# Performance work log

Measured on AMD Instinct MI355X. Metric: run time of the kernel, lower is better.

The kernel has to match this reference:

```python
import jax, jax.numpy as jnp
import numpy as np

B, N, E, HD, L, LH, NC = 256, 96, 1024, 300, 2, 600, 7

def prelu(x, a):
    return jnp.where(x >= 0, x, a * x)

def setup_inputs():
    key = jax.random.key(0)
    ks = jax.random.split(key, 16)
    s = 0.02
    r = lambda i, shp: jax.random.normal(ks[i], shp, jnp.float32) * s
    z = lambda shp: jnp.zeros(shp, jnp.float32)
    GD = HD * (L + 1)
    inp = {}
    inp["features"] = jax.random.normal(ks[0], (B, N, E), jnp.float32)
    inp["s_mask"] = jax.random.randint(ks[1], (B, N, N), 0, 2, jnp.int32)
    inp["entro"] = jax.random.uniform(ks[2], (B, N), dtype=jnp.float32)
    inp["alpha"] = 0.5
    inp["threshold"] = 0.25
    inp["fc1_w"] = r(3, (HD, E)); inp["fc1_b"] = z((HD,))
    inp["gat_w"] = r(4, (L, 2 * HD)); inp["gat_b"] = z((L,))
    inp["wr0"] = r(5, (L, HD, HD)); inp["wr1"] = r(6, (L, HD, HD))
    inp["enhance_w"] = r(7, (E, E)); inp["enhance_b"] = z((E,))
    inp["prelu_a"] = jnp.array(0.25, jnp.float32)
    inp["lstm_w_ih"] = r(8, (4 * LH, E + GD)); inp["lstm_w_hh"] = r(9, (4 * LH, LH))
    inp["lstm_b_ih"] = z((4 * LH,)); inp["lstm_b_hh"] = z((4 * LH,))
    inp["mlp_w0"] = r(10, (HD, LH)); inp["mlp_b0"] = z((HD,)); inp["mlp_a0"] = jnp.array(0.25, jnp.float32)
    inp["mlp_w1"] = r(11, (HD, HD)); inp["mlp_b1"] = z((HD,)); inp["mlp_a1"] = jnp.array(0.25, jnp.float32)
    inp["out_w"] = r(12, (NC, HD)); inp["out_b"] = z((NC,))
    return inp

def reference(features, s_mask, entro, alpha, threshold, fc1_w, fc1_b, gat_w, gat_b, wr0, wr1, enhance_w, enhance_b, prelu_a, lstm_w_ih, lstm_w_hh, lstm_b_ih, lstm_b_hh, mlp_w0, mlp_b0, mlp_a0, mlp_w1, mlp_b1, mlp_a1, out_w, out_b):
    # context_filter: cosine similarity + entropy edge filtering -> binary adjacency (B,N,N)
    f = features / (jnp.linalg.norm(features, axis=-1, keepdims=True) + 1e-8)
    sim = jnp.einsum("bid,bjd->bij", f, f)
    comb = alpha * entro[:, None, :] + (1.0 - alpha) * sim
    adj = comb > threshold
    H0 = prelu(features @ fc1_w.T + fc1_b, prelu_a)
    sm = s_mask.astype(features.dtype)
    Hs = [H0]
    for l in range(L):
        Hl = Hs[-1]
        wq, wk = gat_w[l, :HD], gat_w[l, HD:]
        # fused GAT over all target nodes i: score[b,i,j] = wq.H[b,i] + wk.H[b,j] + b
        scores = (Hl @ wq)[:, :, None] + (Hl @ wk)[:, None, :] + gat_b[l]
        scores = jnp.where(adj, scores, -1e9)
        attn = jax.nn.softmax(scores, axis=-1)
        V0 = Hl @ wr0[l].T  # relation-0 transform
        V1 = Hl @ wr1[l].T  # relation-1 transform
        M = jnp.einsum("bij,bjd->bid", attn * sm, V0) + jnp.einsum("bij,bjd->bid", attn * (1.0 - sm), V1)
        Hs.append(M)
    Hcat = jnp.concatenate(Hs, axis=2)  # (B, N, HD*(L+1))
    feat = prelu(features @ enhance_w.T + enhance_b, prelu_a)
    seq = jnp.concatenate([feat, Hcat], axis=-1)
    zin = seq @ lstm_w_ih.T + lstm_b_ih + lstm_b_hh  # (B, N, 4*LH), input projection hoisted out of scan
    def step(carry, zt):
        h, c = carry
        g = zt + h @ lstm_w_hh.T
        i, fg, gg, o = jnp.split(g, 4, axis=-1)
        c = jax.nn.sigmoid(fg) * c + jax.nn.sigmoid(i) * jnp.tanh(gg)
        h = jax.nn.sigmoid(o) * jnp.tanh(c)
        return (h, c), h
    h0 = jnp.zeros((features.shape[0], LH), features.dtype)
    _, hs = jax.lax.scan(step, (h0, h0), jnp.swapaxes(zin, 0, 1))
    Hl = jnp.swapaxes(hs, 0, 1)  # (B, N, LH)
    x = prelu(Hl @ mlp_w0.T + mlp_b0, mlp_a0)
    x = prelu(x @ mlp_w1.T + mlp_b1, mlp_a1)
    return x @ out_w.T + out_b  # (B, N, NC)
```

## Files before the change

### kernel.cpp

```cpp
#include <hip/hip_runtime.h>
#include <cstdint>
#include <cstddef>

#define Bdim 256
#define Ndim 96
#define Edim 1024
#define HDdim 300
#define Ldim 2
#define LHdim 600
#define NCdim 7
#define GDdim 900
#define ROWS (Bdim*Ndim)
#define HSLICE 155648

typedef unsigned short u16;
typedef unsigned int   u32;
typedef float f32x4 __attribute__((ext_vector_type(4)));
typedef short bf16x8 __attribute__((ext_vector_type(8)));
typedef unsigned short u16x4 __attribute__((ext_vector_type(4)));

#define IDP 0x7FFFFFFF, 1, 30, 0, 0

__device__ inline u16 f2bf(float x) {
    u32 u = __builtin_bit_cast(u32, x);
    u32 r = (u + 0x7fffu + ((u >> 16) & 1u)) >> 16;
    return (u16)r;
}
__device__ inline float bf2f(u16 h) {
    u32 u = ((u32)h) << 16;
    return __builtin_bit_cast(float, u);
}

template<int OUT, int ACT>
__global__ __launch_bounds__(256) void gemm_bf16(
    const u16* __restrict__ Ah, int lda,
    const u16* __restrict__ Wh, int ldw,
    float* __restrict__ C, u16* __restrict__ Ch, int ldc,
    int M, int Nd, int K,
    const float* __restrict__ bias, const float* __restrict__ aptr)
{
    __shared__ u16 At[2][4][1024];
    __shared__ u16 Wt[2][4][1024];
    const int tid  = threadIdx.x;
    const int ny  = gridDim.y;
    const int nwg = gridDim.x * ny;
    const int lin = blockIdx.y * gridDim.x + blockIdx.x;
    const int q = nwg >> 3, r8 = nwg & 7;
    const int xcd = lin & 7, off = lin >> 3;
    const int swz = (xcd < r8) ? xcd * (q + 1) + off
                               : r8 * (q + 1) + (xcd - r8) * q + off;
    const int bm   = (swz / ny) * 128;
    const int bn   = (swz % ny) * 128;
    const int wv   = tid >> 6;
    const int lane = tid & 63;
    const int wr   = (wv >> 1) * 64;
    const int wc   = (wv & 1) * 64;
    const int l15  = lane & 15;
    const int kseg = lane >> 4;

    f32x4 acc[4][4];
    #pragma unroll
    for (int i = 0; i < 4; ++i)
        #pragma unroll
        for (int j = 0; j < 4; ++j) acc[i][j] = (f32x4){0.f,0.f,0.f,0.f};

    const int srow = tid & 127;
    const bool isA = (tid < 128);
    const int gr   = isA ? (bm + srow) : (bn + srow);
    const u16* pbase = (isA ? Ah : Wh) + (size_t)gr * (isA ? lda : ldw);
    u16* dst = isA ? &At[0][0][0] : &Wt[0][0][0];
    const int soff = srow * 8;

    bf16x8 rv[4];
    #pragma unroll
    for (int s = 0; s < 4; ++s) rv[s] = *(const bf16x8*)(pbase + s * 8);

    const int nk = K >> 5;
    for (int kc = 0; kc < nk; ++kc) {
        const int bufo = (kc & 1) << 12;
        #pragma unroll
        for (int s = 0; s < 4; ++s)
            *(bf16x8*)(dst + bufo + s * 1024 + soff) = rv[s];
        if (kc + 1 < nk) {
            const u16* p = pbase + (kc + 1) * 32;
            #pragma unroll
            for (int s = 0; s < 4; ++s) rv[s] = *(const bf16x8*)(p + s * 8);
        }
        __syncthreads();
        const u16* Ab = &At[0][0][0] + bufo + kseg * 1024;
        const u16* Wb = &Wt[0][0][0] + bufo + kseg * 1024;
        bf16x8 a[4], b[4];
        #pragma unroll
        for (int f = 0; f < 4; ++f) {
            a[f] = *(const bf16x8*)(Ab + (wr + f * 16 + l15) * 8);
            b[f] = *(const bf16x8*)(Wb + (wc + f * 16 + l15) * 8);
        }
        #pragma unroll
        for (int i = 0; i < 4; ++i)
            #pragma unroll
            for (int j = 0; j < 4; ++j)
                acc[i][j] = __builtin_amdgcn_mfma_f32_16x16x32_bf16(a[i], b[j], acc[i][j], 0, 0, 0);
    }

    const float av = (ACT == 1) ? *aptr : 0.f;
    const int r4 = (lane >> 4) * 4;
    #pragma unroll
    for (int j = 0; j < 4; ++j) {
        int col = bn + wc + j * 16 + l15;
        if (col >= Nd) continue;
        float bv = bias ? bias[col] : 0.f;
        #pragma unroll
        for (int i = 0; i < 4; ++i) {
            #pragma unroll
            for (int rr = 0; rr < 4; ++rr) {
                int row = bm + wr + i * 16 + r4 + rr;
                if (row >= M) continue;
                float v = acc[i][j][rr] + bv;
                if (ACT == 1) v = (v >= 0.f) ? v : av * v;
                if (OUT == 0) {
                    C[(size_t)row * ldc + col] = v;
                } else {
                    Ch[(size_t)row * ldc + col] = f2bf(v);
                }
            }
        }
    }
}

__global__ __launch_bounds__(256) void split_rows8(
    const float* __restrict__ src, int srcld,
    int pmask, int pmul1, int pshift, int pmul2, int padd,
    u16* __restrict__ dstH, int dstld,
    int wcols, int validK, int validRows)
{
    const int r = blockIdx.y * 4 + (threadIdx.x >> 6);
    const int c = (blockIdx.x * 64 + (threadIdx.x & 63)) * 8;
    if (c >= wcols) return;
    const int sr = (r & pmask) * pmul1 + (r >> pshift) * pmul2 + padd;
    const float* s = src + (size_t)sr * srcld;
    const bool rok = (r < validRows);
    float v[8];
    if (rok && c + 8 <= validK) {
        *(float4*)&v[0] = *(const float4*)(s + c);
        *(float4*)&v[4] = *(const float4*)(s + c + 4);
    } else {
        #pragma unroll
        for (int u = 0; u < 8; ++u) v[u] = (rok && c + u < validK) ? s[c + u] : 0.f;
    }
    bf16x8 H8;
    #pragma unroll
    for (int u = 0; u < 8; ++u) H8[u] = (short)f2bf(v[u]);
    *(bf16x8*)(dstH + (size_t)r * dstld + c) = H8;
}

__global__ __launch_bounds__(256) void bias_perm(
    const float* __restrict__ bih, const float* __restrict__ bhh, float* __restrict__ dst)
{
    int n = blockIdx.x * 256 + threadIdx.x;
    if (n >= 4 * LHdim) return;
    int o = (n & 3) * LHdim + (n >> 2);
    dst[n] = bih[o] + bhh[o];
}

__global__ __launch_bounds__(256) void wr_cat(
    const float* __restrict__ wr0, const float* __restrict__ wr1, float* __restrict__ dst)
{
    int c = blockIdx.x * 256 + threadIdx.x;
    if (c >= HDdim) return;
    int lr = blockIdx.y;
    int l = lr / (2 * HDdim), r = lr % (2 * HDdim);
    const float* src = (r < HDdim)
        ? wr0 + ((size_t)l * HDdim + r) * HDdim
        : wr1 + ((size_t)l * HDdim + (r - HDdim)) * HDdim;
    dst[(size_t)lr * HDdim + c] = src[c];
}

__global__ __launch_bounds__(256) void zero_range(float* __restrict__ p, int n)
{
    int i = blockIdx.x * 256 + threadIdx.x;
    if (i < n) p[i] = 0.f;
}

__global__ __launch_bounds__(256) void norm_kernel(const float* __restrict__ f, float* __restrict__ invn)
{
    int row  = blockIdx.x * 4 + (threadIdx.x >> 6);
    int lane = threadIdx.x & 63;
    const float* fr = f + (size_t)row * Edim;
    float ss = 0.f;
    for (int t = lane; t < Edim; t += 64) { float v = fr[t]; ss = fmaf(v, v, ss); }
    #pragma unroll
    for (int o = 32; o > 0; o >>= 1) ss += __shfl_down(ss, o);
    if (lane == 0) invn[row] = 1.f / (sqrtf(ss) + 1e-8f);
}

__global__ __launch_bounds__(256) void simadj_kernel(
    const float* __restrict__ f, const float* __restrict__ invn,
    const float* __restrict__ entro, const float* __restrict__ alphap,
    const float* __restrict__ thrp, uint8_t* __restrict__ adj)
{
    int b = blockIdx.x;
    __shared__ float S[16][100];
    int tid = threadIdx.x;
    int i0 = (tid >> 4) * 6, j0 = (tid & 15) * 6;
    float acc[6][6];
    #pragma unroll
    for (int i = 0; i < 6; ++i)
        #pragma unroll
        for (int j = 0; j < 6; ++j) acc[i][j] = 0.f;
    const float* fb = f + (size_t)b * Ndim * Edim;

    for (int k0 = 0; k0 < Edim; k0 += 16) {
        __syncthreads();
        #pragma unroll
        for (int r = 0; r < 6; ++r) {
            int n = (tid >> 4) + r * 16;
            S[tid & 15][n] = fb[(size_t)n * Edim + k0 + (tid & 15)];
        }
        __syncthreads();
        #pragma unroll
        for (int kk = 0; kk < 16; ++kk) {
            float a[6], bb[6];
            #pragma unroll
            for (int u = 0; u < 6; ++u) a[u] = S[kk][i0 + u];
            #pragma unroll
            for (int u = 0; u < 6; ++u) bb[u] = S[kk][j0 + u];
            #pragma unroll
            for (int i = 0; i < 6; ++i)
                #pragma unroll
                for (int j = 0; j < 6; ++j)
                    acc[i][j] = fmaf(a[i], bb[j], acc[i][j]);
        }
    }

    float alpha = *alphap, thr = *thrp;
    float onem = 1.f - alpha;
    #pragma unroll
    for (int i = 0; i < 6; ++i) {
        int ii = i0 + i;
        float inv_i = invn[b * Ndim + ii];
        #pragma unroll
        for (int j = 0; j < 6; ++j) {
            int jj = j0 + j;
            float simv = acc[i][j] * inv_i * invn[b * Ndim + jj];
            float comb = alpha * entro[b * Ndim + jj] + onem * simv;
            adj[((size_t)b * Ndim + ii) * Ndim + jj] = (comb > thr) ? 1 : 0;
        }
    }
}

__global__ __launch_bounds__(256) void k_kernel(
    const float* __restrict__ Hsrc, const float* __restrict__ wk,
    float* __restrict__ k)
{
    int row  = blockIdx.x * 4 + (threadIdx.x >> 6);
    int lane = threadIdx.x & 63;
    const float* h = Hsrc + (size_t)row * GDdim;
    float sk = 0.f;
    for (int t = lane; t < HDdim; t += 64) sk = fmaf(h[t], wk[t], sk);
    #pragma unroll
    for (int o = 32; o > 0; o >>= 1) sk += __shfl_down(sk, o);
    if (lane == 0) k[row] = sk;
}

__global__ __launch_bounds__(256) void gat_fused(
    const float* __restrict__ kbuf, const uint8_t* __restrict__ adj,
    const int* __restrict__ smask,
    const float* __restrict__ V,
    float* __restrict__ Mout)
{
    __shared__ u16 P0[96][100];
    __shared__ u16 P1[96][100];
    __shared__ u16 Vs0[96][96];
    __shared__ u16 Vs1[96][96];
    __shared__ float ek[96];
    __shared__ float rden[96];
    __shared__ float red[256];
    const int b = blockIdx.x;
    const int half = blockIdx.y;
    const int tid = threadIdx.x;

    float kj = (tid < Ndim) ? kbuf[tid * Bdim + b] : -1e30f;
    red[tid] = kj;
    __syncthreads();
    #pragma unroll
    for (int s = 128; s > 0; s >>= 1) {
        if (tid < s) red[tid] = fmaxf(red[tid], red[tid + s]);
        __syncthreads();
    }
    float kmax = red[0];
    if (tid < Ndim) ek[tid] = expf(kj - kmax);
    __syncthreads();
    if (tid < Ndim) {
        const uint8_t* ar = adj + ((size_t)b * Ndim + tid) * Ndim;
        float s = 0.f;
        for (int j = 0; j < Ndim; ++j) if (ar[j]) s += ek[j];
        rden[tid] = 1.f / s;
    }
    __syncthreads();
    for (int idx = tid; idx < Ndim * Ndim; idx += 256) {
        int i = idx / Ndim, j = idx - i * Ndim;
        float a = adj[((size_t)b * Ndim + i) * Ndim + j] ? ek[j] * rden[i] : 0.f;
        int s = smask[((size_t)b * Ndim + i) * Ndim + j];
        P0[i][j] = s ? f2bf(a) : (u16)0;
        P1[i][j] = s ? (u16)0 : f2bf(a);
    }
    __syncthreads();

    const int ti = tid >> 4, td = tid & 15;
    const int i0 = ti * 6, dbase = td * 6;
    for (int p = 2 * half; p < 2 * half + 2; ++p) {
        const int d0 = p * 96;
        const int dw = (p == 3) ? (HDdim - 288) : 96;
        for (int idx = tid; idx < 96 * 24; idx += 256) {
            int j = idx / 24, q4 = (idx - j * 24) * 4;
            if (q4 < dw) {
                size_t g = ((size_t)(j * Bdim + b)) * (2 * HDdim) + d0 + q4;
                float4 a = *(const float4*)(V + g);
                float4 c = *(const float4*)(V + g + HDdim);
                u16x4 ua = { f2bf(a.x), f2bf(a.y), f2bf(a.z), f2bf(a.w) };
                u16x4 uc = { f2bf(c.x), f2bf(c.y), f2bf(c.z), f2bf(c.w) };
                *(u16x4*)&Vs0[j][q4] = ua;
                *(u16x4*)&Vs1[j][q4] = uc;
            }
        }
        __syncthreads();
        float acc[6][6];
        #pragma unroll
        for (int ii = 0; ii < 6; ++ii)
            #pragma unroll
            for (int dd = 0; dd < 6; ++dd) acc[ii][dd] = 0.f;
        for (int j = 0; j < Ndim; j += 2) {
            float paj[6], pajn[6], pbj[6], pbjn[6];
            #pragma unroll
            for (int ii = 0; ii < 6; ++ii) {
                u32 w0 = *(const u32*)&P0[i0 + ii][j];
                u32 w1 = *(const u32*)&P1[i0 + ii][j];
                paj[ii]  = __builtin_bit_cast(float, w0 << 16);
                pajn[ii] = __builtin_bit_cast(float, w0 & 0xffff0000u);
                pbj[ii]  = __builtin_bit_cast(float, w1 << 16);
                pbjn[ii] = __builtin_bit_cast(float, w1 & 0xffff0000u);
            }
            float v0a[6], v0b[6], v1a[6], v1b[6];
            #pragma unroll
            for (int dd = 0; dd < 3; ++dd) {
                u32 wa = *(const u32*)&Vs0[j][dbase + 2 * dd];
                u32 wb = *(const u32*)&Vs0[j + 1][dbase + 2 * dd];
                u32 wc2 = *(const u32*)&Vs1[j][dbase + 2 * dd];
                u32 wd = *(const u32*)&Vs1[j + 1][dbase + 2 * dd];
                v0a[2*dd]   = __builtin_bit_cast(float, wa << 16);
                v0a[2*dd+1] = __builtin_bit_cast(float, wa & 0xffff0000u);
                v0b[2*dd]   = __builtin_bit_cast(float, wb << 16);
                v0b[2*dd+1] = __builtin_bit_cast(float, wb & 0xffff0000u);
                v1a[2*dd]   = __builtin_bit_cast(float, wc2 << 16);
                v1a[2*dd+1] = __builtin_bit_cast(float, wc2 & 0xffff0000u);
                v1b[2*dd]   = __builtin_bit_cast(float, wd << 16);
                v1b[2*dd+1] = __builtin_bit_cast(float, wd & 0xffff0000u);
            }
            #pragma unroll
            for (int ii = 0; ii < 6; ++ii)
                #pragma unroll
                for (int dd = 0; dd < 6; ++dd) {
                    acc[ii][dd] += paj[ii]  * v0a[dd] + pbj[ii]  * v1a[dd]
                                 + pajn[ii] * v0b[dd] + pbjn[ii] * v1b[dd];
                }
        }
        __syncthreads();
        #pragma unroll
        for (int ii = 0; ii < 6; ++ii) {
            #pragma unroll
            for (int dd = 0; dd < 6; ++dd) {
                int d = dbase + dd;
                if (d < dw)
                    Mout[((size_t)((i0 + ii) * Bdim + b)) * GDdim + d0 + d] = acc[ii][dd];
            }
        }
    }
}

__global__ __launch_bounds__(256) void lstm_bf16(
    const u16* __restrict__ hH,
    const float* __restrict__ cin,
    const u16* __restrict__ WH,
    const float* __restrict__ zt,
    u16* __restrict__ hHo,
    float* __restrict__ cout)
{
    __shared__ u16 As[2][4][256];
    __shared__ u16 Ws[2][4][512];
    __shared__ __align__(16) float gates[32][68];
    const int tid = threadIdx.x;
    const int bm = blockIdx.x * 32;
    const int bn = blockIdx.y * 64;
    const int wv = tid >> 6;
    const int lane = tid & 63;
    const int l15 = lane & 15;
    const int kseg = lane >> 4;
    const float4 fz = make_float4(0.f, 0.f, 0.f, 0.f);

    const int prow0 = tid >> 4,        pui0 = tid & 15;
    const int prow1 = (tid + 256) >> 4, pui1 = tid & 15;
    const int pn0 = bn + pui0 * 4,  pn1 = bn + pui1 * 4;
    const int pu0 = pn0 >> 2,       pu1 = pn1 >> 2;
    const bool ok0 = (pu0 < LHdim), ok1 = (pu1 < LHdim);
    const int bb0 = bm + prow0,     bb1 = bm + prow1;
    float4 z0 = ok0 ? *(const float4*)(zt + (size_t)bb0 * (4 * LHdim) + pn0) : fz;
    float4 z1 = ok1 ? *(const float4*)(zt + (size_t)bb1 * (4 * LHdim) + pn1) : fz;
    float ci0 = ok0 ? cin[bb0 * LHdim + pu0] : 0.f;
    float ci1 = ok1 ? cin[bb1 * LHdim + pu1] : 0.f;

    const int av = tid & 127;
    const int arow = av >> 2, akc = av & 3;
    const u16* asrc = hH + (size_t)(bm + arow) * 608 + akc * 8;
    const int aoff = akc * 256 + arow * 8;
    const bool doA = (tid < 128);
    const int wrow = tid >> 2, wkc = tid & 3;
    const u16* wsrc = WH + (size_t)(bn + wrow) * 608 + wkc * 8;
    const int woff2 = wrow * 8;

    f32x4 acc[2];
    acc[0] = (f32x4){0.f,0.f,0.f,0.f};
    acc[1] = (f32x4){0.f,0.f,0.f,0.f};

    bf16x8 ra = *(const bf16x8*)(asrc);
    bf16x8 rw = *(const bf16x8*)(wsrc);

    #pragma unroll
    for (int kc = 0; kc < 19; ++kc) {
        const int buf = kc & 1;
        if (doA) *(bf16x8*)(&As[buf][0][0] + aoff) = ra;
        *(bf16x8*)(&Ws[buf][wkc][woff2]) = rw;
        if (kc + 1 < 19) {
            ra = *(const bf16x8*)(asrc + (kc + 1) * 32);
            rw = *(const bf16x8*)(wsrc + (kc + 1) * 32);
        }
        __syncthreads();
        bf16x8 a0, a1, b;
        a0 = *(const bf16x8*)&As[buf][kseg][(l15) * 8];
        a1 = *(const bf16x8*)&As[buf][kseg][(16 + l15) * 8];
        b  = *(const bf16x8*)&Ws[buf][kseg][(wv * 16 + l15) * 8];
        acc[0] = __builtin_amdgcn_mfma_f32_16x16x32_bf16(a0, b, acc[0], 0, 0, 0);
        acc[1] = __builtin_amdgcn_mfma_f32_16x16x32_bf16(a1, b, acc[1], 0, 0, 0);
    }

    const int r4 = (lane >> 4) * 4;
    __syncthreads();
    #pragma unroll
    for (int i = 0; i < 2; ++i)
        #pragma unroll
        for (int rr = 0; rr < 4; ++rr)
            gates[i * 16 + r4 + rr][wv * 16 + l15] = acc[i][rr];
    __syncthreads();

    if (ok0) {
        float4 g = *(const float4*)&gates[prow0][pui0 * 4];
        float gi = g.x + z0.x;
        float gf = g.y + z0.y;
        float gg = g.z + z0.z;
        float go = g.w + z0.w;
        float si = 1.f / (1.f + expf(-gi));
        float sf = 1.f / (1.f + expf(-gf));
        float so = 1.f / (1.f + expf(-go));
        float cn = sf * ci0 + si * tanhf(gg);
        float hn = so * tanhf(cn);
        cout[bb0 * LHdim + pu0] = cn;
        hHo[(size_t)bb0 * 608 + pu0] = f2bf(hn);
    }
    if (ok1) {
        float4 g = *(const float4*)&gates[prow1][pui1 * 4];
        float gi = g.x + z1.x;
        float gf = g.y + z1.y;
        float gg = g.z + z1.z;
        float go = g.w + z1.w;
        float si = 1.f / (1.f + expf(-gi));
        float sf = 1.f / (1.f + expf(-gf));
        float so = 1.f / (1.f + expf(-go));
        float cn = sf * ci1 + si * tanhf(gg);
        float hn = so * tanhf(cn);
        cout[bb1 * LHdim + pu1] = cn;
        hHo[(size_t)bb1 * 608 + pu1] = f2bf(hn);
    }
}

__global__ __launch_bounds__(256) void out_kernel(
    const float* __restrict__ x, int ldx, const float* __restrict__ ow,
    const float* __restrict__ ob, float* __restrict__ out)
{
    int r    = blockIdx.x * 4 + (threadIdx.x >> 6);
    int lane = threadIdx.x & 63;
    const float* xr = x + (size_t)r * ldx;
    float acc[NCdim];
    #pragma unroll
    for (int n = 0; n < NCdim; ++n) acc[n] = 0.f;
    for (int t = lane; t < HDdim; t += 64) {
        float xv = xr[t];
        #pragma unroll
        for (int n = 0; n < NCdim; ++n) acc[n] = fmaf(xv, ow[n * HDdim + t], acc[n]);
    }
    #pragma unroll
    for (int o = 32; o > 0; o >>= 1)
        #pragma unroll
        for (int n = 0; n < NCdim; ++n) acc[n] += __shfl_down(acc[n], o);
    if (lane == 0) {
        int b = r & 255, nn = r >> 8;
        #pragma unroll
        for (int n = 0; n < NCdim; ++n) out[((size_t)b * Ndim + nn) * NCdim + n] = acc[n] + ob[n];
    }
}

extern "C" void kernel_launch(void* const* d_in, const int* in_sizes, int n_in,
                              void* d_out, int out_size, void* d_ws, size_t ws_size,
                              hipStream_t stream)
{
    const float*  features  = (const float*)d_in[0];
    const int*    s_mask    = (const int*)  d_in[1];
    const float*  entro     = (const float*)d_in[2];
    const float*  alpha     = (const float*)d_in[3];
    const float*  threshold = (const float*)d_in[4];
    const float*  fc1_w     = (const float*)d_in[5];
    const float*  fc1_b     = (const float*)d_in[6];
    const float*  gat_w     = (const float*)d_in[7];
    const float*  gat_b     = (const float*)d_in[8];
    const float*  wr0       = (const float*)d_in[9];
    const float*  wr1       = (const float*)d_in[10];
    const float*  enhance_w = (const float*)d_in[11];
    const float*  enhance_b = (const float*)d_in[12];
    const float*  prelu_a   = (const float*)d_in[13];
    const float*  lstm_w_ih = (const float*)d_in[14];
    const float*  lstm_w_hh = (const float*)d_in[15];
    const float*  lstm_b_ih = (const float*)d_in[16];
    const float*  lstm_b_hh = (const float*)d_in[17];
    const float*  mlp_w0    = (const float*)d_in[18];
    const float*  mlp_b0    = (const float*)d_in[19];
    const float*  mlp_a0    = (const float*)d_in[20];
    const float*  mlp_w1    = (const float*)d_in[21];
    const float*  mlp_b1    = (const float*)d_in[22];
    const float*  mlp_a1    = (const float*)d_in[23];
    const float*  out_w     = (const float*)d_in[24];
    const float*  out_b     = (const float*)d_in[25];
    float* out = (float*)d_out;
    char* ws = (char*)d_ws;
    (void)gat_b;

    uint8_t* adj   = (uint8_t*)(ws + 0);
    float*   invn  = (float*)(ws + 2359296);
    float*   kbuf  = (float*)(ws + 2457600);
    float*   biasP = (float*)(ws + 2555904);
    float*   c0    = (float*)(ws + 2566144);
    float*   c1    = (float*)(ws + 3180544);
    u16*     WhhPH = (u16*)(ws + 3794944);
    u16*     WihPH = (u16*)(ws + 6752256);
    u16*     EwH   = (u16*)(ws + 16246784);
    u16*     Fc1H  = (u16*)(ws + 18343936);
    float*   Wr2f  = (float*)(ws + 19130368);
    u16*     Wr2H  = (u16*)(ws + 20570368);
    u16*     Wm0H  = (u16*)(ws + 21389568);
    u16*     Wm1H  = (u16*)(ws + 21856512);
    u16*     FfH   = (u16*)(ws + 22102272);
    float*   Hcat  = (float*)(ws + 72433920);
    u16*     HsH   = (u16*)(ws + 160907520);
    float*   V      = (float*)(ws + 176636160);
    u16*     HlstmH = (u16*)(ws + 176636160);
    u16*     x1H   = (u16*)Hcat;
    float*   x2    = (float*)(ws + 72433920 + 31457280);

    const size_t fixedNeed = 235618560ull;
    const size_t perT = 3457024ull;
    int T;
    if      (ws_size >= fixedNeed + 96ull * perT) T = 96;
    else if (ws_size >= fixedNeed + 48ull * perT) T = 48;
    else if (ws_size >= fixedNeed + 32ull * perT) T = 32;
    else if (ws_size >= fixedNeed + 16ull * perT) T = 16;
    else if (ws_size >= fixedNeed +  8ull * perT) T = 8;
    else return;
    char* cr = ws + fixedNeed;
    float* zin  = (float*)cr;
    u16*   seqH = (u16*)(cr + (size_t)T * 2457600);

    norm_kernel<<<ROWS / 4, 256, 0, stream>>>(features, invn);
    simadj_kernel<<<Bdim, 256, 0, stream>>>(features, invn, entro, alpha, threshold, adj);

    split_rows8<<<dim3(2, ROWS / 4), 256, 0, stream>>>(
        features, Edim, 255, Ndim, 8, 1, 0, FfH, Edim, Edim, Edim, ROWS);
    split_rows8<<<dim3(2, 96), 256, 0, stream>>>(
        fc1_w, Edim, IDP, Fc1H, Edim, Edim, Edim, HDdim);
    split_rows8<<<dim3(2, 256), 256, 0, stream>>>(
        enhance_w, Edim, IDP, EwH, Edim, Edim, Edim, Edim);
    split_rows8<<<dim3(4, 608), 256, 0, stream>>>(
        lstm_w_ih, Edim + GDdim, 3, LHdim, 2, 1, 0, WihPH, 1952, 1952, 1924, 2400);
    split_rows8<<<dim3(2, 608), 256, 0, stream>>>(
        lstm_w_hh, LHdim, 3, LHdim, 2, 1, 0, WhhPH, 608, 608, LHdim, 2400);
    split_rows8<<<dim3(2, 96), 256, 0, stream>>>(
        mlp_w0, LHdim, IDP, Wm0H, 608, 608, LHdim, HDdim);
    split_rows8<<<dim3(1, 96), 256, 0, stream>>>(
        mlp_w1, HDdim, IDP, Wm1H, 320, 320, HDdim, HDdim);
    wr_cat<<<dim3(2, 2 * Ldim * HDdim), 256, 0, stream>>>(wr0, wr1, Wr2f);
    for (int l = 0; l < Ldim; ++l)
        split_rows8<<<dim3(1, 160), 256, 0, stream>>>(
            Wr2f + (size_t)l * 2 * HDdim * HDdim, HDdim, IDP,
            Wr2H + (size_t)l * 640 * 320, 320, 320, HDdim, 2 * HDdim);
    bias_perm<<<10, 256, 0, stream>>>(lstm_b_ih, lstm_b_hh, biasP);
    zero_range<<<1200, 256, 0, stream>>>(c0, 307200);

    gemm_bf16<0,1><<<dim3(ROWS/128, 3), 256, 0, stream>>>(
        FfH, Edim, Fc1H, Edim,
        Hcat, nullptr, GDdim, ROWS, HDdim, Edim, fc1_b, prelu_a);

    for (int l = 0; l < Ldim; ++l) {
        const float* Hsrc = Hcat + l * HDdim;
        k_kernel<<<ROWS / 4, 256, 0, stream>>>(Hsrc, gat_w + l * 2 * HDdim + HDdim, kbuf);
        split_rows8<<<dim3(1, ROWS / 4), 256, 0, stream>>>(
            Hsrc, GDdim, IDP, HsH, 320, 320, HDdim, ROWS);
        gemm_bf16<0,0><<<dim3(ROWS/128, 5), 256, 0, stream>>>(
            HsH, 320, Wr2H + (size_t)l * 640 * 320, 320,
            V, nullptr, 2 * HDdim, ROWS, 2 * HDdim, 320, nullptr, nullptr);
        gat_fused<<<dim3(Bdim, 2), 256, 0, stream>>>(
            kbuf, adj, s_mask, V, Hcat + (l + 1) * HDdim);
    }

    zero_range<<<29489, 256, 0, stream>>>((float*)HlstmH, 7548928);

    int cur = 0;
    float* cb_[2] = {c0, c1};
    for (int t0 = 0; t0 < Ndim; t0 += T) {
        int Mc = T * Bdim;
        gemm_bf16<1,1><<<dim3(Mc/128, 8), 256, 0, stream>>>(
            FfH + (size_t)t0 * Bdim * Edim, Edim, EwH, Edim,
            nullptr, seqH, 1952, Mc, Edim, Edim, enhance_b, prelu_a);
        split_rows8<<<dim3(2, Mc / 4), 256, 0, stream>>>(
            Hcat, GDdim, 0x7FFFFFFF, 1, 30, 0, t0 * Bdim,
            seqH + 1024, 1952, 928, GDdim, Mc);
        gemm_bf16<0,0><<<dim3(Mc/128, 19), 256, 0, stream>>>(
            seqH, 1952, WihPH, 1952,
            zin, nullptr, 4 * LHdim, Mc, 4 * LHdim, 1952, biasP, nullptr);
        for (int tl = 0; tl < T; ++tl) {
            const int g = t0 + tl;
            lstm_bf16<<<dim3(8, 38), 256, 0, stream>>>(
                HlstmH + (size_t)g * HSLICE, cb_[cur], WhhPH,
                zin + (size_t)tl * Bdim * 4 * LHdim,
                HlstmH + (size_t)(g + 1) * HSLICE, cb_[cur ^ 1]);
            cur ^= 1;
        }
    }

    zero_range<<<15360, 256, 0, stream>>>((float*)x1H, 3932160);
    gemm_bf16<1,1><<<dim3(ROWS/128, 3), 256, 0, stream>>>(
        HlstmH + HSLICE, 608, Wm0H, 608,
        nullptr, x1H, 320, ROWS, HDdim, 608, mlp_b0, mlp_a0);
    gemm_bf16<0,1><<<dim3(ROWS/128, 3), 256, 0, stream>>>(
        x1H, 320, Wm1H, 320,
        x2, nullptr, 304, ROWS, HDdim, 320, mlp_b1, mlp_a1);
    out_kernel<<<ROWS / 4, 256, 0, stream>>>(x2, 304, out_w, out_b, out);
}
```

Measured before the change: 2.437 ms.

## Load full K-range of LSTM recurrent GEMM into LDS with 64x64 tiles

The per-timestep LSTM recurrent kernel now uses 64x64 output tiles per block, with a 2x2 MFMA arrangement per wave, instead of 32x64. It stages the whole K dimension of both h and W_hh into about 152KB of shared memory in one batched load phase, replacing the 19-step double-buffered loop that synchronised every step. This halves the grid to 4x38 blocks and cuts barrier count and W_hh reloads per row. In exchange there are fewer blocks, so less parallelism across the GPU's CUs, and the large LDS footprint allows only one block per CU.

```diff
diff --git a/kernel.cpp b/kernel.cpp
--- a/kernel.cpp
+++ b/kernel.cpp
@@ -377,7 +377,7 @@
     }
 }
 
-__global__ __launch_bounds__(256) void lstm_bf16(
+__global__ __launch_bounds__(256) void lstm_fused(
     const u16* __restrict__ hH,
     const float* __restrict__ cin,
     const u16* __restrict__ WH,
@@ -385,99 +385,98 @@
     u16* __restrict__ hHo,
     float* __restrict__ cout)
 {
-    __shared__ u16 As[2][4][256];
-    __shared__ u16 Ws[2][4][512];
-    __shared__ __align__(16) float gates[32][68];
+    __shared__ u16 AW[2][38912];
     const int tid = threadIdx.x;
-    const int bm = blockIdx.x * 32;
+    const int bm = blockIdx.x * 64;
     const int bn = blockIdx.y * 64;
     const int wv = tid >> 6;
     const int lane = tid & 63;
     const int l15 = lane & 15;
     const int kseg = lane >> 4;
-    const float4 fz = make_float4(0.f, 0.f, 0.f, 0.f);
-
-    const int prow0 = tid >> 4,        pui0 = tid & 15;
-    const int prow1 = (tid + 256) >> 4, pui1 = tid & 15;
-    const int pn0 = bn + pui0 * 4,  pn1 = bn + pui1 * 4;
-    const int pu0 = pn0 >> 2,       pu1 = pn1 >> 2;
-    const bool ok0 = (pu0 < LHdim), ok1 = (pu1 < LHdim);
-    const int bb0 = bm + prow0,     bb1 = bm + prow1;
-    float4 z0 = ok0 ? *(const float4*)(zt + (size_t)bb0 * (4 * LHdim) + pn0) : fz;
-    float4 z1 = ok1 ? *(const float4*)(zt + (size_t)bb1 * (4 * LHdim) + pn1) : fz;
-    float ci0 = ok0 ? cin[bb0 * LHdim + pu0] : 0.f;
-    float ci1 = ok1 ? cin[bb1 * LHdim + pu1] : 0.f;
-
-    const int av = tid & 127;
-    const int arow = av >> 2, akc = av & 3;
-    const u16* asrc = hH + (size_t)(bm + arow) * 608 + akc * 8;
-    const int aoff = akc * 256 + arow * 8;
-    const bool doA = (tid < 128);
-    const int wrow = tid >> 2, wkc = tid & 3;
-    const u16* wsrc = WH + (size_t)(bn + wrow) * 608 + wkc * 8;
-    const int woff2 = wrow * 8;
-
-    f32x4 acc[2];
-    acc[0] = (f32x4){0.f,0.f,0.f,0.f};
-    acc[1] = (f32x4){0.f,0.f,0.f,0.f};
-
-    bf16x8 ra = *(const bf16x8*)(asrc);
-    bf16x8 rw = *(const bf16x8*)(wsrc);
-
-    #pragma unroll
-    for (int kc = 0; kc < 19; ++kc) {
-        const int buf = kc & 1;
-        if (doA) *(bf16x8*)(&As[buf][0][0] + aoff) = ra;
-        *(bf16x8*)(&Ws[buf][wkc][woff2]) = rw;
-        if (kc + 1 < 19) {
-            ra = *(const bf16x8*)(asrc + (kc + 1) * 32);
-            rw = *(const bf16x8*)(wsrc + (kc + 1) * 32);
-        }
-        __syncthreads();
-        bf16x8 a0, a1, b;
-        a0 = *(const bf16x8*)&As[buf][kseg][(l15) * 8];
-        a1 = *(const bf16x8*)&As[buf][kseg][(16 + l15) * 8];
-        b  = *(const bf16x8*)&Ws[buf][kseg][(wv * 16 + l15) * 8];
-        acc[0] = __builtin_amdgcn_mfma_f32_16x16x32_bf16(a0, b, acc[0], 0, 0, 0);
-        acc[1] = __builtin_amdgcn_mfma_f32_16x16x32_bf16(a1, b, acc[1], 0, 0, 0);
-    }
-
+    const int wr2 = (wv >> 1) * 32;
+    const int wc2 = (wv & 1) * 32;
+
+    float4 z[4]; float ci[4]; bool ok[4]; int bb[4], pu[4];
+    #pragma unroll
+    for (int k = 0; k < 4; ++k) {
+        int c4 = k * 256 + tid;
+        int row = c4 >> 4, u = c4 & 15;
+        bb[k] = bm + row;
+        pu[k] = (bn >> 2) + u;
+        ok[k] = (pu[k] < LHdim);
+        z[k] = ok[k] ? *(const float4*)(zt + (size_t)bb[k] * (4 * LHdim) + bn + u * 4)
+                     : make_float4(0.f, 0.f, 0.f, 0.f);
+        ci[k] = ok[k] ? cin[bb[k] * LHdim + pu[k]] : 0.f;
+    }
+
+    const int srow = tid >> 2, sks = tid & 3;
+    const u16* ag = hH + (size_t)(bm + srow) * 608 + sks * 8;
+    const u16* wg = WH + (size_t)(bn + srow) * 608 + sks * 8;
+    u16* al = &AW[0][(sks * 64 + srow) * 8];
+    u16* wl = &AW[1][(sks * 64 + srow) * 8];
+    #pragma unroll
+    for (int cb = 0; cb < 20; cb += 4) {
+        bf16x8 ra[4], rw[4];
+        #pragma unroll
+        for (int c = 0; c < 4; ++c)
+            if (cb + c < 19) {
+                ra[c] = *(const bf16x8*)(ag + (cb + c) * 32);
+                rw[c] = *(const bf16x8*)(wg + (cb + c) * 32);
+            }
+        #pragma unroll
+        for (int c = 0; c < 4; ++c)
+            if (cb + c < 19) {
+                *(bf16x8*)(al + (cb + c) * 2048) = ra[c];
+                *(bf16x8*)(wl + (cb + c) * 2048) = rw[c];
+            }
+    }
+    __syncthreads();
+
+    f32x4 acc[2][2];
+    acc[0][0] = acc[0][1] = acc[1][0] = acc[1][1] = (f32x4){0.f,0.f,0.f,0.f};
+    const u16* Ab = &AW[0][kseg * 512];
+    const u16* Wb = &AW[1][kseg * 512];
+    #pragma unroll
+    for (int c = 0; c < 19; ++c) {
+        bf16x8 a0 = *(const bf16x8*)(Ab + c * 2048 + (wr2 + l15) * 8);
+        bf16x8 a1 = *(const bf16x8*)(Ab + c * 2048 + (wr2 + 16 + l15) * 8);
+        bf16x8 b0 = *(const bf16x8*)(Wb + c * 2048 + (wc2 + l15) * 8);
+        bf16x8 b1 = *(const bf16x8*)(Wb + c * 2048 + (wc2 + 16 + l15) * 8);
+        acc[0][0] = __builtin_amdgcn_mfma_f32_16x16x32_bf16(a0, b0, acc[0][0], 0, 0, 0);
+        acc[0][1] = __builtin_amdgcn_mfma_f32_16x16x32_bf16(a0, b1, acc[0][1], 0, 0, 0);
+        acc[1][0] = __builtin_amdgcn_mfma_f32_16x16x32_bf16(a1, b0, acc[1][0], 0, 0, 0);
+        acc[1][1] = __builtin_amdgcn_mfma_f32_16x16x32_bf16(a1, b1, acc[1][1], 0, 0, 0);
+    }
+
+    __syncthreads();
+    float* gates = (float*)&AW[0][0];
     const int r4 = (lane >> 4) * 4;
+    #pragma unroll
+    for (int i = 0; i < 2; ++i)
+        #pragma unroll
+        for (int j = 0; j < 2; ++j)
+            #pragma unroll
+            for (int rr = 0; rr < 4; ++rr)
+                gates[(wr2 + i * 16 + r4 + rr) * 68 + wc2 + j * 16 + l15] = acc[i][j][rr];
     __syncthreads();
-    #pragma unroll
-    for (int i = 0; i < 2; ++i)
-        #pragma unroll
-        for (int rr = 0; rr < 4; ++rr)
-            gates[i * 16 + r4 + rr][wv * 16 + l15] = acc[i][rr];
-    __syncthreads();
-
-    if (ok0) {
-        float4 g = *(const float4*)&gates[prow0][pui0 * 4];
-        float gi = g.x + z0.x;
-        float gf = g.y + z0.y;
-        float gg = g.z + z0.z;
-        float go = g.w + z0.w;
+
+    #pragma unroll
+    for (int k = 0; k < 4; ++k) {
+        if (!ok[k]) continue;
+        int c4 = k * 256 + tid;
+        int row = c4 >> 4, u = c4 & 15;
+        float4 g = *(const float4*)&gates[row * 68 + u * 4];
+        float gi = g.x + z[k].x;
+        float gf = g.y + z[k].y;
+        float gg = g.z + z[k].z;
+        float go = g.w + z[k].w;
         float si = 1.f / (1.f + expf(-gi));
         float sf = 1.f / (1.f + expf(-gf));
         float so = 1.f / (1.f + expf(-go));
-        float cn = sf * ci0 + si * tanhf(gg);
+        float cn = sf * ci[k] + si * tanhf(gg);
         float hn = so * tanhf(cn);
-        cout[bb0 * LHdim + pu0] = cn;
-        hHo[(size_t)bb0 * 608 + pu0] = f2bf(hn);
-    }
-    if (ok1) {
-        float4 g = *(const float4*)&gates[prow1][pui1 * 4];
-        float gi = g.x + z1.x;
-        float gf = g.y + z1.y;
-        float gg = g.z + z1.z;
-        float go = g.w + z1.w;
-        float si = 1.f / (1.f + expf(-gi));
-        float sf = 1.f / (1.f + expf(-gf));
-        float so = 1.f / (1.f + expf(-go));
-        float cn = sf * ci1 + si * tanhf(gg);
-        float hn = so * tanhf(cn);
-        cout[bb1 * LHdim + pu1] = cn;
-        hHo[(size_t)bb1 * 608 + pu1] = f2bf(hn);
+        cout[bb[k] * LHdim + pu[k]] = cn;
+        hHo[(size_t)bb[k] * 608 + pu[k]] = f2bf(hn);
     }
 }
 
@@ -634,7 +633,7 @@
             zin, nullptr, 4 * LHdim, Mc, 4 * LHdim, 1952, biasP, nullptr);
         for (int tl = 0; tl < T; ++tl) {
             const int g = t0 + tl;
-            lstm_bf16<<<dim3(8, 38), 256, 0, stream>>>(
+            lstm_fused<<<dim3(4, 38), 256, 0, stream>>>(
                 HlstmH + (size_t)g * HSLICE, cb_[cur], WhhPH,
                 zin + (size_t)tl * Bdim * 4 * LHdim,
                 HlstmH + (size_t)(g + 1) * HSLICE, cb_[cur ^ 1]);
```

Result: faster. 2.188 ms (-10.2%).
